# Performance work log

Hardware: AMD Instinct MI355X
Metric: run time of the kernel (lower is better)

## Reference

```python
import jax, jax.numpy as jnp
import numpy as np

B, S = 16, 32            # batch, cfg.feature_samples
CF, CC, H, W = 768, 512, 28, 28
NEG = 2                  # cfg.neg_samples
POS_INTRA_SHIFT, POS_INTER_SHIFT, NEG_INTER_SHIFT = 0.18, 0.12, 0.46


def _norm(t):
    # F.normalize(t, dim=1, eps=1e-10)
    n = jnp.sqrt(jnp.sum(t * t, axis=1, keepdims=True))
    return t / jnp.maximum(n, 1e-10)


def _grid_sample(img, grid):
    # torch F.grid_sample, bilinear, padding_mode='border', align_corners=True
    # img [B,C,H,W], grid [B,Hg,Wg,2] with (x,y) in [-1,1]
    Hh, Ww = img.shape[2], img.shape[3]
    x = (grid[..., 0] + 1.0) * 0.5 * (Ww - 1)
    y = (grid[..., 1] + 1.0) * 0.5 * (Hh - 1)
    x0 = jnp.floor(x); y0 = jnp.floor(y)
    wx = x - x0; wy = y - y0
    x0c = jnp.clip(x0, 0, Ww - 1).astype(jnp.int32)
    x1c = jnp.clip(x0 + 1, 0, Ww - 1).astype(jnp.int32)
    y0c = jnp.clip(y0, 0, Hh - 1).astype(jnp.int32)
    y1c = jnp.clip(y0 + 1, 0, Hh - 1).astype(jnp.int32)
    gather = jax.vmap(lambda im, yy, xx: im[:, yy, xx])  # -> [B,C,Hg,Wg]
    Ia, Ib = gather(img, y0c, x0c), gather(img, y1c, x0c)
    Ic, Id = gather(img, y0c, x1c), gather(img, y1c, x1c)
    wx = wx[:, None]; wy = wy[:, None]
    return Ia * (1 - wx) * (1 - wy) + Ib * (1 - wx) * wy + Ic * wx * (1 - wy) + Id * wx * wy


def _sample(t, coords):
    # sample(): grid_sample(t, coords.permute(0,2,1,3))
    return _grid_sample(t, jnp.transpose(coords, (0, 2, 1, 3)))


def _corr(a, b):
    return jnp.einsum('nchw,ncij->nhwij', a, b)


def _helper(f1, f2, c1, c2, shift):
    # fd computed under no_grad in torch
    fd = jax.lax.stop_gradient(_corr(_norm(f1), _norm(f2)))
    # cfg.pointwise = True
    old_mean = fd.mean()
    fd = fd - fd.mean(axis=(3, 4), keepdims=True)
    fd = fd - fd.mean() + old_mean
    cd = _corr(_norm(c1), _norm(c2))
    # cfg.zero_clamp=True, cfg.stabalize=False -> cd.clamp(0.0)
    return -jnp.maximum(cd, 0.0) * (fd - shift)


def setup_inputs() -> dict:
    key = jax.random.key(0)
    ks = jax.random.split(key, 11)
    return {
        'orig_feats': jax.random.normal(ks[0], (B, CF, H, W), jnp.float32),
        'orig_feats_pos': jax.random.normal(ks[1], (B, CF, H, W), jnp.float32),
        'orig_salience': jax.random.uniform(ks[2], (B, 224, 224), jnp.float32),
        'orig_salience_pos': jax.random.uniform(ks[3], (B, 224, 224), jnp.float32),
        'orig_code': jax.random.normal(ks[4], (B, CC, H, W), jnp.float32),
        'orig_code_pos': jax.random.normal(ks[5], (B, CC, H, W), jnp.float32),
        'depth': jax.random.uniform(ks[6], (B, 1, 224, 224), jnp.float32),
        'depth_pos': jax.random.uniform(ks[7], (B, 1, 224, 224), jnp.float32),
        'coords1': jax.random.uniform(ks[8], (B, S, S, 2), jnp.float32),
        'coords2': jax.random.uniform(ks[9], (B, S, S, 2), jnp.float32),
        'perms': jax.random.randint(ks[10], (NEG, B), 0, B, jnp.int32),
    }


def reference(orig_feats, orig_feats_pos, orig_salience, orig_salience_pos,
              orig_code, orig_code_pos, depth, depth_pos,
              coords1, coords2, perms):
    # random-coordinate branch: coords = rand(...) * 2 - 1
    c1 = coords1 * 2.0 - 1.0
    c2 = coords2 * 2.0 - 1.0
    feats = _sample(orig_feats, c1)
    code = _sample(orig_code, c1)
    feats_pos = _sample(orig_feats_pos, c2)
    code_pos = _sample(orig_code_pos, c2)

    pos_intra = _helper(feats, feats, code, code, POS_INTRA_SHIFT).mean()
    pos_inter = _helper(feats, feats_pos, code, code_pos, POS_INTER_SHIFT).mean()

    def neg_one(perm):
        feats_neg = _sample(orig_feats[perm], c2)
        code_neg = _sample(orig_code[perm], c2)
        return _helper(feats, feats_neg, code, code_neg, NEG_INTER_SHIFT).mean()

    neg_inter = jax.vmap(neg_one)(perms).mean()
    return jnp.stack([pos_intra, pos_inter, neg_inter])
```

## Files before the change

kernel.cpp:

```cpp
#include <hip/hip_runtime.h>
#include <hip/hip_bf16.h>

#define NB 16
#define NP 1024
#define CF 768
#define CC 512
#define HH 28
#define WW 28
#define HW 784
#define NTOT 16777216.0f

typedef float f32x4 __attribute__((ext_vector_type(4)));
struct __align__(8) bf4 { __hip_bfloat16 a, b, c, d; };

__device__ __forceinline__ float b2f(__hip_bfloat16 h) { return __bfloat162float(h); }


__global__ void transpose_bf16_kernel(const float* __restrict__ in0,
                                      const float* __restrict__ in1,
                                      __hip_bfloat16* __restrict__ out, int C) {
  __shared__ float tile[32][33];
  int p0 = blockIdx.x * 32, c0 = blockIdx.y * 32;
  int t = blockIdx.z >> 4, b = blockIdx.z & 15;
  int tx = threadIdx.x, ty = threadIdx.y;
  const float* ib = (t == 0 ? in0 : in1) + (size_t)b * C * HW;
  __hip_bfloat16* ob = out + ((size_t)t * NB + b) * HW * C;
#pragma unroll
  for (int i = 0; i < 32; i += 8) {
    int c = c0 + ty + i, p = p0 + tx;
    if (p < HW) tile[ty + i][tx] = ib[(size_t)c * HW + p];
  }
  __syncthreads();
#pragma unroll
  for (int i = 0; i < 32; i += 8) {
    int p = p0 + ty + i, c = c0 + tx;
    if (p < HW) ob[(size_t)p * C + c] = __float2bfloat16(tile[tx][ty + i]);
  }
}

__global__ __launch_bounds__(256) void sample_pack_kernel(
    const __hip_bfloat16* __restrict__ fTb, const __hip_bfloat16* __restrict__ cTb,
    const float* __restrict__ coords1, const float* __restrict__ coords2,
    const int* __restrict__ perms,
    unsigned char* __restrict__ Fb, unsigned char* __restrict__ Cb,
    float* __restrict__ scF, float* __restrict__ scC) {
  __shared__ int offs[4][64];
  __shared__ float wts[4][64];
  __shared__ char tile[4160];

  int bb = blockIdx.y, slot = blockIdx.z;
  int tid = threadIdx.x;
  int p0 = blockIdx.x * 64;
  int pt = blockIdx.x >> 1, mh = blockIdx.x & 1;

  const float* coords = (slot == 0) ? coords1 : coords2;
  int srcidx;
  if (slot == 0)      srcidx = bb;
  else if (slot == 1) srcidx = 16 + bb;
  else if (slot == 2) srcidx = perms[bb];
  else                srcidx = perms[16 + bb];

  if (tid < 64) {
    int p = p0 + tid;
    float cx = coords[((size_t)bb * NP + p) * 2 + 0];
    float cy = coords[((size_t)bb * NP + p) * 2 + 1];
    float x = cx * (WW - 1), y = cy * (HH - 1);
    float x0f = floorf(x), y0f = floorf(y);
    float wx = x - x0f, wy = y - y0f;
    int x0 = min(max((int)x0f, 0), WW - 1);
    int x1 = min(max((int)x0f + 1, 0), WW - 1);
    int y0 = min(max((int)y0f, 0), HH - 1);
    int y1 = min(max((int)y0f + 1, 0), HH - 1);
    offs[0][tid] = y0 * WW + x0;
    offs[1][tid] = y1 * WW + x0;
    offs[2][tid] = y0 * WW + x1;
    offs[3][tid] = y1 * WW + x1;
    wts[0][tid] = (1.f - wx) * (1.f - wy);
    wts[1][tid] = (1.f - wx) * wy;
    wts[2][tid] = wx * (1.f - wy);
    wts[3][tid] = wx * wy;
  }
  __syncthreads();

  int gid = tid >> 4, l = tid & 15;
  int r = l >> 1, h4 = l & 1;

  {
    const __hip_bfloat16* base = fTb + (size_t)srcidx * HW * CF;
    float ssq[4] = {0.f, 0.f, 0.f, 0.f};
    for (int kt = 0; kt < 12; ++kt) {
#pragma unroll
      for (int j = 0; j < 4; ++j) {
        int m = j * 16 + gid;
        float4 v = {0.f, 0.f, 0.f, 0.f};
#pragma unroll
        for (int c = 0; c < 4; ++c) {
          const bf4 t4 = *((const bf4*)(base + (size_t)offs[c][m] * CF) + kt * 16 + l);
          float wv = wts[c][m];
          v.x += wv * b2f(t4.a); v.y += wv * b2f(t4.b);
          v.z += wv * b2f(t4.c); v.w += wv * b2f(t4.d);
        }
        ssq[j] += v.x * v.x + v.y * v.y + v.z * v.z + v.w * v.w;
        int w0 = __builtin_amdgcn_cvt_pk_fp8_f32(v.x, v.y, 0, false);
        int w1 = __builtin_amdgcn_cvt_pk_fp8_f32(v.z, v.w, w0, true);
        *(int*)(tile + r * 520 + m * 8 + h4 * 4) = w1;
      }
      __syncthreads();
      unsigned char* gbase = Fb +
          (((((size_t)slot * NB + bb) * 12 + kt) * 8 + pt) * 1024 + (size_t)mh * 64) * 8;
#pragma unroll
      for (int jj = 0; jj < 2; ++jj) {
        int cl = jj * 256 + tid;
        int rr = cl >> 6, mi = cl & 63;
        unsigned long long val = *(const unsigned long long*)(tile + rr * 520 + mi * 8);
        *(unsigned long long*)(gbase + (size_t)(rr * 128 + mi) * 8) = val;
      }
      __syncthreads();
    }
#pragma unroll
    for (int j = 0; j < 4; ++j) {
#pragma unroll
      for (int mm = 1; mm < 16; mm <<= 1) ssq[j] += __shfl_xor(ssq[j], mm);
    }
    if (l == 0) {
#pragma unroll
      for (int j = 0; j < 4; ++j) {
        int p = p0 + j * 16 + gid;
        scF[((size_t)slot * NB + bb) * NP + p] = 1.f / fmaxf(sqrtf(ssq[j]), 1e-10f);
      }
    }
  }

  {
    const __hip_bfloat16* base = cTb + (size_t)srcidx * HW * CC;
    float ssq[4] = {0.f, 0.f, 0.f, 0.f};
    for (int kt = 0; kt < 8; ++kt) {
#pragma unroll
      for (int j = 0; j < 4; ++j) {
        int m = j * 16 + gid;
        float4 v = {0.f, 0.f, 0.f, 0.f};
#pragma unroll
        for (int c = 0; c < 4; ++c) {
          const bf4 t4 = *((const bf4*)(base + (size_t)offs[c][m] * CC) + kt * 16 + l);
          float wv = wts[c][m];
          v.x += wv * b2f(t4.a); v.y += wv * b2f(t4.b);
          v.z += wv * b2f(t4.c); v.w += wv * b2f(t4.d);
        }
        ssq[j] += v.x * v.x + v.y * v.y + v.z * v.z + v.w * v.w;
        int w0 = __builtin_amdgcn_cvt_pk_fp8_f32(v.x, v.y, 0, false);
        int w1 = __builtin_amdgcn_cvt_pk_fp8_f32(v.z, v.w, w0, true);
        *(int*)(tile + r * 520 + m * 8 + h4 * 4) = w1;
      }
      __syncthreads();
      unsigned char* gbase = Cb +
          (((((size_t)slot * NB + bb) * 8 + kt) * 8 + pt) * 1024 + (size_t)mh * 64) * 8;
#pragma unroll
      for (int jj = 0; jj < 2; ++jj) {
        int cl = jj * 256 + tid;
        int rr = cl >> 6, mi = cl & 63;
        unsigned long long val = *(const unsigned long long*)(tile + rr * 520 + mi * 8);
        *(unsigned long long*)(gbase + (size_t)(rr * 128 + mi) * 8) = val;
      }
      __syncthreads();
    }
#pragma unroll
    for (int j = 0; j < 4; ++j) {
#pragma unroll
      for (int mm = 1; mm < 16; mm <<= 1) ssq[j] += __shfl_xor(ssq[j], mm);
    }
    if (l == 0) {
#pragma unroll
      for (int j = 0; j < 4; ++j) {
        int p = p0 + j * 16 + gid;
        scC[((size_t)slot * NB + bb) * NP + p] = 1.f / fmaxf(sqrtf(ssq[j]), 1e-10f);
      }
    }
  }
}

__device__ __forceinline__ void stage_sup(const unsigned long long* __restrict__ st,
                                          unsigned long long* buf, int tid) {
#pragma unroll
  for (int i = 0; i < 2; ++i) {
    const char* g = (const char*)st + (size_t)(i * 256 + tid) * 16;
    char* d = (char*)buf + i * 4096 + (tid & 192) * 16;
    __builtin_amdgcn_global_load_lds(
        (const __attribute__((address_space(1))) void*)g,
        (__attribute__((address_space(3))) void*)d, 16, 0, 0);
  }
}

__device__ __forceinline__ void mfma_tile(const unsigned long long* __restrict__ A,
                                          const unsigned long long* __restrict__ B,
                                          int aoff, int boff, f32x4 acc[4][4]) {
#pragma unroll
  for (int s = 0; s < 2; ++s) {
    long a[4], b[4];
#pragma unroll
    for (int mi = 0; mi < 4; ++mi) a[mi] = (long)A[s * 512 + aoff + mi * 16];
#pragma unroll
    for (int ni = 0; ni < 4; ++ni) b[ni] = (long)B[s * 512 + boff + ni * 16];
#pragma unroll
    for (int mi = 0; mi < 4; ++mi)
#pragma unroll
      for (int ni = 0; ni < 4; ++ni)
        acc[mi][ni] = __builtin_amdgcn_mfma_f32_16x16x32_fp8_fp8(
            a[mi], b[ni], acc[mi][ni], 0, 0, 0);
  }
}

#define WAITV(N) asm volatile("s_waitcnt vmcnt(" #N ")" ::: "memory")
#define BAR() do { __builtin_amdgcn_s_barrier(); \
                   __builtin_amdgcn_sched_barrier(0); } while (0)

__global__ __launch_bounds__(256, 2) void corr_kernel(
    const unsigned long long* __restrict__ Fb,
    const unsigned long long* __restrict__ Cb,
    const float* __restrict__ scF, const float* __restrict__ scC,
    float* __restrict__ rowfd, float* __restrict__ rowrcd,
    float* __restrict__ cross) {
  __shared__ unsigned long long Afs[2][1024], Bfs[2][1024],
                                Acs[2][1024], Bcs[2][1024];

  int id = blockIdx.x;
  int zl = id & 7, q = id >> 3;
  int bx = q & 7, by = (q >> 3) & 7, zh = q >> 6;
  int z = zh * 8 + zl;
  int h = z >> 4, bb = z & 15;
  int p0 = bx * 128, q0 = by * 128;
  int tid = threadIdx.x, ln = tid & 63, w = tid >> 6;
  int wm = w >> 1, wn = w & 1, quad = ln >> 4, t16 = ln & 15;
  int aoff = quad * 128 + wm * 64 + t16;
  int boff = quad * 128 + wn * 64 + t16;

  const unsigned long long* AfB = Fb + (((size_t)bb * 12) * 8 + bx) * 1024;
  const unsigned long long* BfB = Fb + ((((size_t)h * NB + bb) * 12) * 8 + by) * 1024;
  const unsigned long long* AcB = Cb + (((size_t)bb * 8) * 8 + bx) * 1024;
  const unsigned long long* BcB = Cb + ((((size_t)h * NB + bb) * 8) * 8 + by) * 1024;
  const size_t KTSTR = (size_t)8 * 1024;

  f32x4 accf[4][4], accc[4][4];
#pragma unroll
  for (int i = 0; i < 4; ++i)
#pragma unroll
    for (int j = 0; j < 4; ++j) {
      accf[i][j] = (f32x4){0.f, 0.f, 0.f, 0.f};
      accc[i][j] = (f32x4){0.f, 0.f, 0.f, 0.f};
    }

  stage_sup(AfB, Afs[0], tid);
  stage_sup(BfB, Bfs[0], tid);
  stage_sup(AcB, Acs[0], tid);
  stage_sup(BcB, Bcs[0], tid);
  stage_sup(AfB + KTSTR, Afs[1], tid);
  stage_sup(BfB + KTSTR, Bfs[1], tid);

#pragma unroll
  for (int kt = 0; kt < 12; ++kt) {
    const int cur = kt & 1, nxt = cur ^ 1;
    if (kt >= 1 && kt < 11) {
      stage_sup(AfB + (size_t)(kt + 1) * KTSTR, Afs[nxt], tid);
      stage_sup(BfB + (size_t)(kt + 1) * KTSTR, Bfs[nxt], tid);
    }
    if (kt <= 7)       { WAITV(8); }
    else if (kt <= 10) { WAITV(4); }
    else               { WAITV(0); }
    BAR();
    __builtin_amdgcn_s_setprio(1);
    mfma_tile(Afs[cur], Bfs[cur], aoff, boff, accf);
    __builtin_amdgcn_s_setprio(0);
    if (kt < 8) {
      if (kt < 7) {
        stage_sup(AcB + (size_t)(kt + 1) * KTSTR, Acs[nxt], tid);
        stage_sup(BcB + (size_t)(kt + 1) * KTSTR, Bcs[nxt], tid);
      }
      if (kt <= 6) { WAITV(8); } else { WAITV(4); }
      BAR();
      __builtin_amdgcn_s_setprio(1);
      mfma_tile(Acs[cur], Bcs[cur], aoff, boff, accc);
      __builtin_amdgcn_s_setprio(0);
    }
  }

  float* sm = (float*)Afs;
  {
    const float* s0 = scF + (size_t)bb * NP;
    const float* s1 = scF + ((size_t)h * NB + bb) * NP;
    const float* s2 = scC + (size_t)bb * NP;
    const float* s3 = scC + ((size_t)h * NB + bb) * NP;
    if (tid < 128) {
      sm[tid] = s0[p0 + tid];
      sm[256 + tid] = s2[p0 + tid];
    } else {
      int u = tid - 128;
      sm[128 + u] = s1[q0 + u];
      sm[384 + u] = s3[q0 + u];
    }
  }
  __syncthreads();

  float sbf[4], sbc[4];
#pragma unroll
  for (int ni = 0; ni < 4; ++ni) {
    int qq = wn * 64 + ni * 16 + t16;
    sbf[ni] = sm[128 + qq];
    sbc[ni] = sm[384 + qq];
  }
  float cross_l = 0.f;
#pragma unroll
  for (int mi = 0; mi < 4; ++mi) {
#pragma unroll
    for (int r = 0; r < 4; ++r) {
      int pl = wm * 64 + mi * 16 + quad * 4 + r;
      float saf = sm[pl], sac = sm[256 + pl];
      float sfd = 0.f, srw = 0.f;
#pragma unroll
      for (int ni = 0; ni < 4; ++ni) {
        float fd = accf[mi][ni][r] * (saf * sbf[ni]);
        float cd = accc[mi][ni][r] * (sac * sbc[ni]);
        float rc = fmaxf(cd, 0.f);
        sfd += fd;
        srw += rc;
        cross_l += rc * fd;
      }
#pragma unroll
      for (int mm = 1; mm < 16; mm <<= 1) {
        sfd += __shfl_xor(sfd, mm);
        srw += __shfl_xor(srw, mm);
      }
      if (t16 == 0) {
        int p = p0 + pl;
        size_t idx = ((size_t)h * NB + bb) * NP + p;
        atomicAdd(&rowfd[idx], sfd);
        atomicAdd(&rowrcd[idx], srw);
      }
    }
  }
#pragma unroll
  for (int mm = 1; mm < 64; mm <<= 1) cross_l += __shfl_xor(cross_l, mm);
  float* crs = (float*)Bfs;
  if (ln == 0) crs[w] = cross_l;
  __syncthreads();
  if (tid == 0) atomicAdd(&cross[h], crs[0] + crs[1] + crs[2] + crs[3]);
}

__global__ void finalize_partial(const float* __restrict__ rowfd,
                                 const float* __restrict__ rowrcd,
                                 const float* __restrict__ cross,
                                 float* __restrict__ losses) {
  __shared__ float r1[16], r2[16], r3[16];
  const float shifts[4] = {0.18f, 0.12f, 0.46f, 0.46f};
  int h = blockIdx.x, tid = threadIdx.x, w = tid >> 6, ln = tid & 63;
  float s1 = 0.f, s2 = 0.f, s3 = 0.f;
  for (int i = tid; i < NB * NP; i += 1024) {
    float a = rowfd[h * NB * NP + i];
    float c = rowrcd[h * NB * NP + i];
    s1 += a;
    s2 += c;
    s3 += a * c;
  }
#pragma unroll
  for (int mm = 1; mm < 64; mm <<= 1) {
    s1 += __shfl_xor(s1, mm);
    s2 += __shfl_xor(s2, mm);
    s3 += __shfl_xor(s3, mm);
  }
  if (ln == 0) { r1[w] = s1; r2[w] = s2; r3[w] = s3; }
  __syncthreads();
  if (tid == 0) {
    float Sfd = 0.f, Srcd = 0.f, Sdot = 0.f;
#pragma unroll
    for (int i = 0; i < 16; ++i) { Sfd += r1[i]; Srcd += r2[i]; Sdot += r3[i]; }
    losses[h] = -(cross[h] - Sdot * (1.0f / 1024.0f) +
                  (Sfd / NTOT - shifts[h]) * Srcd) / NTOT;
  }
}

__global__ void finalize_combine(const float* __restrict__ losses,
                                 float* __restrict__ out) {
  if (threadIdx.x == 0) {
    out[0] = losses[0];
    out[1] = losses[1];
    out[2] = 0.5f * (losses[2] + losses[3]);
  }
}

extern "C" void kernel_launch(void* const* d_in, const int* in_sizes, int n_in,
                              void* d_out, int out_size, void* d_ws, size_t ws_size,
                              hipStream_t stream) {
  (void)in_sizes; (void)n_in; (void)out_size; (void)ws_size;
  const float* orig_feats = (const float*)d_in[0];
  const float* orig_feats_pos = (const float*)d_in[1];
  const float* orig_code = (const float*)d_in[4];
  const float* orig_code_pos = (const float*)d_in[5];
  const float* coords1 = (const float*)d_in[8];
  const float* coords2 = (const float*)d_in[9];
  const int* perms = (const int*)d_in[10];
  float* out = (float*)d_out;

  char* ws = (char*)d_ws;
  size_t off = 0;
  __hip_bfloat16* fTb = (__hip_bfloat16*)(ws + off); off += (size_t)2 * NB * HW * CF * 2;
  __hip_bfloat16* cTb = (__hip_bfloat16*)(ws + off); off += (size_t)2 * NB * HW * CC * 2;
  unsigned char* Fb = (unsigned char*)(ws + off); off += (size_t)4 * NB * NP * CF;
  unsigned char* Cb = (unsigned char*)(ws + off); off += (size_t)4 * NB * NP * CC;
  float* rowfd  = (float*)(ws + off); off += (size_t)4 * NB * NP * 4;
  float* rowrcd = (float*)(ws + off); off += (size_t)4 * NB * NP * 4;
  float* cross  = (float*)(ws + off); off += 64;
  float* losses = (float*)(ws + off); off += 64;
  float* scF    = (float*)(ws + off); off += (size_t)4 * NB * NP * 4;
  float* scC    = (float*)(ws + off); off += (size_t)4 * NB * NP * 4;

  (void)hipMemsetAsync(rowfd, 0, (size_t)4 * NB * NP * 4 * 2 + 128, stream);

  dim3 tb(32, 8);
  transpose_bf16_kernel<<<dim3(25, 24, 32), tb, 0, stream>>>(
      orig_feats, orig_feats_pos, fTb, CF);
  transpose_bf16_kernel<<<dim3(25, 16, 32), tb, 0, stream>>>(
      orig_code, orig_code_pos, cTb, CC);
  sample_pack_kernel<<<dim3(16, 16, 4), 256, 0, stream>>>(
      fTb, cTb, coords1, coords2, perms, Fb, Cb, scF, scC);

  corr_kernel<<<dim3(4096), 256, 0, stream>>>(
      (const unsigned long long*)Fb, (const unsigned long long*)Cb,
      scF, scC, rowfd, rowrcd, cross);
  finalize_partial<<<4, 1024, 0, stream>>>(rowfd, rowrcd, cross, losses);
  finalize_combine<<<1, 64, 0, stream>>>(losses, out);
}
```

Before: 414.6 us.

## Serialize code and feature GEMMs with fp16-packed relu cache to raise occupancy

The fused correlation kernel used to hold two full accumulator sets (feature and code) at once. It now runs the code GEMM first, reduces its clamped row sums, and keeps the clamped values packed as fp16 pairs. It then reuses one accumulator set and shared buffers for the feature GEMM, which frees registers and LDS so launch bounds can go from 2 to 3 blocks per CU. The single double buffer becomes a 3-stage LDS ring, and the fp16 truncation of the clamped values adds some precision loss in the cross term.

```diff
diff --git a/kernel.cpp b/kernel.cpp
--- a/kernel.cpp
+++ b/kernel.cpp
@@ -11,6 +11,7 @@
 #define NTOT 16777216.0f
 
 typedef float f32x4 __attribute__((ext_vector_type(4)));
+typedef __fp16 f16x2 __attribute__((ext_vector_type(2)));
 struct __align__(8) bf4 { __hip_bfloat16 a, b, c, d; };
 
 __device__ __forceinline__ float b2f(__hip_bfloat16 h) { return __bfloat162float(h); }
@@ -213,14 +214,14 @@
 #define BAR() do { __builtin_amdgcn_s_barrier(); \
                    __builtin_amdgcn_sched_barrier(0); } while (0)
 
-__global__ __launch_bounds__(256, 2) void corr_kernel(
+__global__ __launch_bounds__(256, 3) void corr_kernel(
     const unsigned long long* __restrict__ Fb,
     const unsigned long long* __restrict__ Cb,
     const float* __restrict__ scF, const float* __restrict__ scC,
     float* __restrict__ rowfd, float* __restrict__ rowrcd,
     float* __restrict__ cross) {
-  __shared__ unsigned long long Afs[2][1024], Bfs[2][1024],
-                                Acs[2][1024], Bcs[2][1024];
+  __shared__ unsigned long long As[3][1024], Bs[3][1024];
+  __shared__ float sm[512];
 
   int id = blockIdx.x;
   int zl = id & 7, q = id >> 3;
@@ -239,50 +240,6 @@
   const unsigned long long* BcB = Cb + ((((size_t)h * NB + bb) * 8) * 8 + by) * 1024;
   const size_t KTSTR = (size_t)8 * 1024;
 
-  f32x4 accf[4][4], accc[4][4];
-#pragma unroll
-  for (int i = 0; i < 4; ++i)
-#pragma unroll
-    for (int j = 0; j < 4; ++j) {
-      accf[i][j] = (f32x4){0.f, 0.f, 0.f, 0.f};
-      accc[i][j] = (f32x4){0.f, 0.f, 0.f, 0.f};
-    }
-
-  stage_sup(AfB, Afs[0], tid);
-  stage_sup(BfB, Bfs[0], tid);
-  stage_sup(AcB, Acs[0], tid);
-  stage_sup(BcB, Bcs[0], tid);
-  stage_sup(AfB + KTSTR, Afs[1], tid);
-  stage_sup(BfB + KTSTR, Bfs[1], tid);
-
-#pragma unroll
-  for (int kt = 0; kt < 12; ++kt) {
-    const int cur = kt & 1, nxt = cur ^ 1;
-    if (kt >= 1 && kt < 11) {
-      stage_sup(AfB + (size_t)(kt + 1) * KTSTR, Afs[nxt], tid);
-      stage_sup(BfB + (size_t)(kt + 1) * KTSTR, Bfs[nxt], tid);
-    }
-    if (kt <= 7)       { WAITV(8); }
-    else if (kt <= 10) { WAITV(4); }
-    else               { WAITV(0); }
-    BAR();
-    __builtin_amdgcn_s_setprio(1);
-    mfma_tile(Afs[cur], Bfs[cur], aoff, boff, accf);
-    __builtin_amdgcn_s_setprio(0);
-    if (kt < 8) {
-      if (kt < 7) {
-        stage_sup(AcB + (size_t)(kt + 1) * KTSTR, Acs[nxt], tid);
-        stage_sup(BcB + (size_t)(kt + 1) * KTSTR, Bcs[nxt], tid);
-      }
-      if (kt <= 6) { WAITV(8); } else { WAITV(4); }
-      BAR();
-      __builtin_amdgcn_s_setprio(1);
-      mfma_tile(Acs[cur], Bcs[cur], aoff, boff, accc);
-      __builtin_amdgcn_s_setprio(0);
-    }
-  }
-
-  float* sm = (float*)Afs;
   {
     const float* s0 = scF + (size_t)bb * NP;
     const float* s1 = scF + ((size_t)h * NB + bb) * NP;
@@ -297,51 +254,133 @@
       sm[384 + u] = s3[q0 + u];
     }
   }
-  __syncthreads();
-
-  float sbf[4], sbc[4];
-#pragma unroll
-  for (int ni = 0; ni < 4; ++ni) {
-    int qq = wn * 64 + ni * 16 + t16;
-    sbf[ni] = sm[128 + qq];
-    sbc[ni] = sm[384 + qq];
-  }
+  asm volatile("s_waitcnt vmcnt(0) lgkmcnt(0)" ::: "memory");
+  __builtin_amdgcn_sched_barrier(0);
+
+  f32x4 acc[4][4];
+#pragma unroll
+  for (int i = 0; i < 4; ++i)
+#pragma unroll
+    for (int j = 0; j < 4; ++j) acc[i][j] = (f32x4){0.f, 0.f, 0.f, 0.f};
+
+  stage_sup(AcB, As[0], tid);
+  stage_sup(BcB, Bs[0], tid);
+  stage_sup(AcB + KTSTR, As[1], tid);
+  stage_sup(BcB + KTSTR, Bs[1], tid);
+#pragma unroll
+  for (int kt = 0; kt < 8; ++kt) {
+    if (kt < 7) { WAITV(4); } else { WAITV(0); }
+    BAR();
+    if (kt + 2 < 8) {
+      stage_sup(AcB + (size_t)(kt + 2) * KTSTR, As[(kt + 2) % 3], tid);
+      stage_sup(BcB + (size_t)(kt + 2) * KTSTR, Bs[(kt + 2) % 3], tid);
+    }
+    __builtin_amdgcn_s_setprio(1);
+    mfma_tile(As[kt % 3], Bs[kt % 3], aoff, boff, acc);
+    __builtin_amdgcn_s_setprio(0);
+  }
+
+  f16x2 rcp[4][4][2];
+  {
+    float sbc[4];
+#pragma unroll
+    for (int ni = 0; ni < 4; ++ni) sbc[ni] = sm[384 + wn * 64 + ni * 16 + t16];
+#pragma unroll
+    for (int mi = 0; mi < 4; ++mi) {
+      float sac[4], srw[4];
+#pragma unroll
+      for (int r = 0; r < 4; ++r) {
+        sac[r] = sm[256 + wm * 64 + mi * 16 + quad * 4 + r];
+        srw[r] = 0.f;
+      }
+#pragma unroll
+      for (int ni = 0; ni < 4; ++ni) {
+        float rc0 = fmaxf(acc[mi][ni][0] * (sac[0] * sbc[ni]), 0.f);
+        float rc1 = fmaxf(acc[mi][ni][1] * (sac[1] * sbc[ni]), 0.f);
+        float rc2 = fmaxf(acc[mi][ni][2] * (sac[2] * sbc[ni]), 0.f);
+        float rc3 = fmaxf(acc[mi][ni][3] * (sac[3] * sbc[ni]), 0.f);
+        srw[0] += rc0; srw[1] += rc1; srw[2] += rc2; srw[3] += rc3;
+        rcp[mi][ni][0] = __builtin_amdgcn_cvt_pkrtz(rc0, rc1);
+        rcp[mi][ni][1] = __builtin_amdgcn_cvt_pkrtz(rc2, rc3);
+      }
+#pragma unroll
+      for (int r = 0; r < 4; ++r) {
+#pragma unroll
+        for (int mm = 1; mm < 16; mm <<= 1) srw[r] += __shfl_xor(srw[r], mm);
+        if (t16 == 0) {
+          int p = p0 + wm * 64 + mi * 16 + quad * 4 + r;
+          atomicAdd(&rowrcd[((size_t)h * NB + bb) * NP + p], srw[r]);
+        }
+      }
+    }
+  }
+
+#pragma unroll
+  for (int i = 0; i < 4; ++i)
+#pragma unroll
+    for (int j = 0; j < 4; ++j) acc[i][j] = (f32x4){0.f, 0.f, 0.f, 0.f};
+
+  __syncthreads();
+
+  stage_sup(AfB, As[0], tid);
+  stage_sup(BfB, Bs[0], tid);
+  stage_sup(AfB + KTSTR, As[1], tid);
+  stage_sup(BfB + KTSTR, Bs[1], tid);
+#pragma unroll
+  for (int kt = 0; kt < 12; ++kt) {
+    if (kt < 11) { WAITV(4); } else { WAITV(0); }
+    BAR();
+    if (kt + 2 < 12) {
+      stage_sup(AfB + (size_t)(kt + 2) * KTSTR, As[(kt + 2) % 3], tid);
+      stage_sup(BfB + (size_t)(kt + 2) * KTSTR, Bs[(kt + 2) % 3], tid);
+    }
+    __builtin_amdgcn_s_setprio(1);
+    mfma_tile(As[kt % 3], Bs[kt % 3], aoff, boff, acc);
+    __builtin_amdgcn_s_setprio(0);
+  }
+
   float cross_l = 0.f;
-#pragma unroll
-  for (int mi = 0; mi < 4; ++mi) {
-#pragma unroll
-    for (int r = 0; r < 4; ++r) {
-      int pl = wm * 64 + mi * 16 + quad * 4 + r;
-      float saf = sm[pl], sac = sm[256 + pl];
-      float sfd = 0.f, srw = 0.f;
+  {
+    float sbf[4];
+#pragma unroll
+    for (int ni = 0; ni < 4; ++ni) sbf[ni] = sm[128 + wn * 64 + ni * 16 + t16];
+#pragma unroll
+    for (int mi = 0; mi < 4; ++mi) {
+      float saf[4], sfd[4];
+#pragma unroll
+      for (int r = 0; r < 4; ++r) {
+        saf[r] = sm[wm * 64 + mi * 16 + quad * 4 + r];
+        sfd[r] = 0.f;
+      }
 #pragma unroll
       for (int ni = 0; ni < 4; ++ni) {
-        float fd = accf[mi][ni][r] * (saf * sbf[ni]);
-        float cd = accc[mi][ni][r] * (sac * sbc[ni]);
-        float rc = fmaxf(cd, 0.f);
-        sfd += fd;
-        srw += rc;
-        cross_l += rc * fd;
-      }
-#pragma unroll
-      for (int mm = 1; mm < 16; mm <<= 1) {
-        sfd += __shfl_xor(sfd, mm);
-        srw += __shfl_xor(srw, mm);
-      }
-      if (t16 == 0) {
-        int p = p0 + pl;
-        size_t idx = ((size_t)h * NB + bb) * NP + p;
-        atomicAdd(&rowfd[idx], sfd);
-        atomicAdd(&rowrcd[idx], srw);
+        float fd0 = acc[mi][ni][0] * (saf[0] * sbf[ni]);
+        float fd1 = acc[mi][ni][1] * (saf[1] * sbf[ni]);
+        float fd2 = acc[mi][ni][2] * (saf[2] * sbf[ni]);
+        float fd3 = acc[mi][ni][3] * (saf[3] * sbf[ni]);
+        sfd[0] += fd0; sfd[1] += fd1; sfd[2] += fd2; sfd[3] += fd3;
+        cross_l += (float)rcp[mi][ni][0][0] * fd0;
+        cross_l += (float)rcp[mi][ni][0][1] * fd1;
+        cross_l += (float)rcp[mi][ni][1][0] * fd2;
+        cross_l += (float)rcp[mi][ni][1][1] * fd3;
+      }
+#pragma unroll
+      for (int r = 0; r < 4; ++r) {
+#pragma unroll
+        for (int mm = 1; mm < 16; mm <<= 1) sfd[r] += __shfl_xor(sfd[r], mm);
+        if (t16 == 0) {
+          int p = p0 + wm * 64 + mi * 16 + quad * 4 + r;
+          atomicAdd(&rowfd[((size_t)h * NB + bb) * NP + p], sfd[r]);
+        }
       }
     }
   }
 #pragma unroll
   for (int mm = 1; mm < 64; mm <<= 1) cross_l += __shfl_xor(cross_l, mm);
-  float* crs = (float*)Bfs;
-  if (ln == 0) crs[w] = cross_l;
-  __syncthreads();
-  if (tid == 0) atomicAdd(&cross[h], crs[0] + crs[1] + crs[2] + crs[3]);
+  __syncthreads();
+  if (ln == 0) sm[w] = cross_l;
+  __syncthreads();
+  if (tid == 0) atomicAdd(&cross[h], sm[0] + sm[1] + sm[2] + sm[3]);
 }
 
 __global__ void finalize_partial(const float* __restrict__ rowfd,
```

Measured after the change: 424.0 us. +2.3%, slower.
